# Performance work log

Hardware: AMD Instinct MI355X
Metric: run time of the kernel (lower is better)

The kernel has to match this reference:

```python
import jax, jax.numpy as jnp
import numpy as np

B, L, H, N, NB = 16, 4096, 256, 64, 4
EXPAND = 2


def setup_inputs() -> dict:
    key = jax.random.key(0)
    ks = jax.random.split(key, 12)
    def nrm(k, shape, scale):
        return jax.random.normal(k, shape, dtype=jnp.float32) * scale
    inp = {}
    inp["x"] = jax.random.normal(ks[0], (B, L, 1), dtype=jnp.float32)
    # conv stem: Conv1d(1 -> H, kernel 5, pad 2)
    inp["conv_w"] = nrm(ks[1], (H, 1, 5), 1.0 / np.sqrt(5.0))
    inp["conv_b"] = jnp.zeros((H,), jnp.float32)
    # per-block S4 (S4D diagonal kernel) params, stacked over NB blocks
    inp["s4_norm_w"] = jnp.ones((NB, H), jnp.float32)
    inp["s4_norm_b"] = jnp.zeros((NB, H), jnp.float32)
    inp["log_dt"] = (np.log(0.001) + jax.random.uniform(ks[2], (NB, H), dtype=jnp.float32) * (np.log(0.1) - np.log(0.001))).astype(jnp.float32)
    inp["log_A_real"] = jnp.full((NB, H, N), np.log(0.5), jnp.float32)
    inp["A_imag"] = jnp.tile(np.pi * jnp.arange(N, dtype=jnp.float32), (NB, H, 1))
    inp["C_re"] = nrm(ks[3], (NB, H, N), 0.5 ** 0.5)
    inp["C_im"] = nrm(ks[4], (NB, H, N), 0.5 ** 0.5)
    inp["D"] = nrm(ks[5], (NB, H), 1.0)
    # S4 output GLU linear: H -> 2H, then glu -> H
    inp["s4_out_w"] = nrm(ks[6], (NB, 2 * H, H), 1.0 / np.sqrt(H))
    inp["s4_out_b"] = jnp.zeros((NB, 2 * H), jnp.float32)
    # FF block (expand=2)
    inp["ff_norm_w"] = jnp.ones((NB, H), jnp.float32)
    inp["ff_norm_b"] = jnp.zeros((NB, H), jnp.float32)
    inp["ff_w1"] = nrm(ks[7], (NB, EXPAND * H, H), 1.0 / np.sqrt(H))
    inp["ff_b1"] = jnp.zeros((NB, EXPAND * H), jnp.float32)
    inp["ff_w2"] = nrm(ks[8], (NB, H, EXPAND * H), 1.0 / np.sqrt(EXPAND * H))
    inp["ff_b2"] = jnp.zeros((NB, H), jnp.float32)
    return inp


def _ln_ch(x, w, b):
    # LayerNorm over channel dim of x: [B, H, L] (prenorm on transposed layout)
    mu = jnp.mean(x, axis=1, keepdims=True)
    var = jnp.mean((x - mu) ** 2, axis=1, keepdims=True)
    return (x - mu) * jax.lax.rsqrt(var + 1e-5) * w[None, :, None] + b[None, :, None]


def _s4d_kernel(log_dt, log_A_real, A_imag, C_re, C_im, Lk):
    # Diagonal SSM (S4D) convolution kernel, returns [H, Lk]
    dt = jnp.exp(log_dt)                       # [H]
    A = -jnp.exp(log_A_real) + 1j * A_imag     # [H, N]
    dtA = A * dt[:, None]                      # [H, N]
    C = (C_re + 1j * C_im) * (jnp.exp(dtA) - 1.0) / A
    V = jnp.exp(dtA[:, :, None] * jnp.arange(Lk, dtype=jnp.float32))  # [H, N, Lk]
    return 2.0 * jnp.einsum('hn,hnl->hl', C, V).real


def reference(x, conv_w, conv_b, s4_norm_w, s4_norm_b, log_dt, log_A_real, A_imag,
              C_re, C_im, D, s4_out_w, s4_out_b, ff_norm_w, ff_norm_b,
              ff_w1, ff_b1, ff_w2, ff_b2):
    u = jnp.transpose(x, (0, 2, 1))  # [B, 1, L]
    h = jax.lax.conv_general_dilated(u, conv_w, (1,), [(2, 2)],
                                     dimension_numbers=('NCH', 'OIH', 'NCH'))
    h = h + conv_b[None, :, None]    # [B, H, L]
    Lx = h.shape[-1]
    for i in range(NB):
        # --- S4 residual block (prenorm, FFT long conv, D-skip, GELU, GLU out) ---
        z = _ln_ch(h, s4_norm_w[i], s4_norm_b[i])
        k = _s4d_kernel(log_dt[i], log_A_real[i], A_imag[i], C_re[i], C_im[i], Lx)
        zf = jnp.fft.rfft(z, n=2 * Lx)
        kf = jnp.fft.rfft(k, n=2 * Lx)
        y = jnp.fft.irfft(zf * kf[None], n=2 * Lx)[..., :Lx]
        y = y + z * D[i][None, :, None]
        y = jax.nn.gelu(y, approximate=False)
        y2 = jnp.einsum('fh,bhl->bfl', s4_out_w[i], y) + s4_out_b[i][None, :, None]
        a, g = jnp.split(y2, 2, axis=1)
        h = h + a * jax.nn.sigmoid(g)
        # --- FF residual block (prenorm, pointwise MLP expand=2, GELU) ---
        z = _ln_ch(h, ff_norm_w[i], ff_norm_b[i])
        z = jax.nn.gelu(jnp.einsum('fh,bhl->bfl', ff_w1[i], z) + ff_b1[i][None, :, None], approximate=False)
        z = jnp.einsum('hf,bfl->bhl', ff_w2[i], z) + ff_b2[i][None, :, None]
        h = h + z
    return h[:, :, -1]  # [B, H]
```

## Files before the change

### kernel.cpp

```cpp
#include <hip/hip_runtime.h>
#include <math.h>

#define Bq 16
#define Lq 4096
#define Hq 256
#define Nq 64
#define NBq 4
#define F2q 512
#define BLq (Bq*Lq)

typedef __attribute__((ext_vector_type(8))) short short8;
typedef __attribute__((ext_vector_type(4))) float f32x4;

__device__ __forceinline__ unsigned short f2bf(float f){
  unsigned u = __float_as_uint(f);
  u = (u + 0x7fffu + ((u >> 16) & 1u)) >> 16;
  return (unsigned short)u;
}
__device__ __forceinline__ float bf2f(unsigned short u){
  return __uint_as_float(((unsigned)u) << 16);
}
__device__ __forceinline__ float gelu(float x){
  float u = 0.79788456f*x*(1.f + 0.044715f*x*x);
  float t = 1.f - __fdividef(2.f, 1.f + __expf(2.f*fabsf(u)));
  return 0.5f*x*(1.f + copysignf(t, u));
}

__device__ __forceinline__ void stage16(const void* g, void* l){
  __builtin_amdgcn_global_load_lds((const __attribute__((address_space(1))) void*)g,
                                   (__attribute__((address_space(3))) void*)l, 16, 0, 0);
}

__global__ __launch_bounds__(256) void k_convln(const float* __restrict__ x,
    const float* __restrict__ cw, const float* __restrict__ cb,
    float* __restrict__ h, float* __restrict__ mu, float* __restrict__ rstd){
  __shared__ float xs[260];
  __shared__ float cwS[Hq*5];
  __shared__ float cbS[Hq];
  const int b = blockIdx.x >> 4;
  const int l0 = (blockIdx.x & 15) * 256;
  const int tid = threadIdx.x;
  for (int i=tid; i<Hq*5; i+=256) cwS[i] = cw[i];
  cbS[tid] = cb[tid];
  {
    int gl = l0 + tid - 2;
    xs[tid] = (gl>=0 && gl<Lq) ? x[(size_t)b*Lq + gl] : 0.f;
    if (tid < 4){
      int gl2 = l0 + 254 + tid;
      xs[256+tid] = (gl2>=0 && gl2<Lq) ? x[(size_t)b*Lq + gl2] : 0.f;
    }
  }
  __syncthreads();
  float s0=0.f, s1=0.f;
  float* hp = h + (size_t)b*Hq*Lq + l0 + tid;
  for (int c=0;c<Hq;c++){
    float acc = cbS[c];
    #pragma unroll
    for (int k=0;k<5;k++) acc = fmaf(cwS[c*5+k], xs[tid+k], acc);
    hp[(size_t)c*Lq] = acc;
    s0 += acc; s1 = fmaf(acc, acc, s1);
  }
  int col = b*Lq + l0 + tid;
  float m = s0 * (1.0f/256.0f);
  float var = s1*(1.0f/256.0f) - m*m;
  mu[col] = m;
  rstd[col] = rsqrtf(fmaxf(var, 0.f) + 1e-5f);
}

__global__ __launch_bounds__(256) void k_s4pre(const float* __restrict__ log_dt,
    const float* __restrict__ lar, const float* __restrict__ aim,
    const float* __restrict__ cre, const float* __restrict__ cim,
    float* __restrict__ wre, float* __restrict__ wim,
    float* __restrict__ c2re, float* __restrict__ c2im){
  int idx = blockIdx.x*256 + threadIdx.x;
  int hh = (idx >> 6) & (Hq-1);
  int i = idx >> 14;
  float dt = expf(log_dt[i*Hq + hh]);
  float are = -expf(lar[idx]);
  float ai  = aim[idx];
  float dre = are*dt, dim = ai*dt;
  float er = expf(dre);
  float wr = er*cosf(dim), wi = er*sinf(dim);
  float nr = wr - 1.f, ni = wi;
  float den = are*are + ai*ai;
  float qre = (nr*are + ni*ai)/den;
  float qim = (ni*are - nr*ai)/den;
  float Cr = cre[idx], Ci = cim[idx];
  float cer = Cr*qre - Ci*qim;
  float cei = Cr*qim + Ci*qre;
  wre[idx] = wr; wim[idx] = wi;
  c2re[idx] = 2.f*cer; c2im[idx] = 2.f*cei;
}

__global__ __launch_bounds__(256) void k_cvtw(const float* __restrict__ s0,
    const float* __restrict__ s1, const float* __restrict__ s2,
    unsigned short* __restrict__ d0, unsigned short* __restrict__ d1,
    unsigned short* __restrict__ d2){
  int idx = blockIdx.x*256 + threadIdx.x;
  d0[idx] = f2bf(s0[idx]);
  d1[idx] = f2bf(s1[idx]);
  d2[idx] = f2bf(s2[idx]);
}

__global__ __launch_bounds__(64) void k_s4mat(const float* __restrict__ wre_,
    const float* __restrict__ wim_, const float* __restrict__ c2re_,
    const float* __restrict__ c2im_, const float* __restrict__ Dp,
    unsigned short* __restrict__ G, unsigned short* __restrict__ Wb,
    float* __restrict__ w64re_, float* __restrict__ w64im_){
  __shared__ float Kv[64];
  const int n = threadIdx.x;
  const int ch = blockIdx.x;
  const int pidx = ch*64 + n;
  const float wr = wre_[pidx], wi = wim_[pidx];
  const float cr = c2re_[pidx], ci = c2im_[pidx];
  unsigned short* Gb = G + (size_t)ch*64*192;
  unsigned short* Wbb = Wb + (size_t)ch*128*64;
  float pre = 1.f, pim = 0.f;
  for (int t=0;t<64;t++){
    float a = cr*pre - ci*pim;
    #pragma unroll
    for (int m=1;m<64;m<<=1) a += __shfl_xor(a, m, 64);
    if (n==0) Kv[t] = a;
    Wbb[n*64 + (63-t)] = f2bf(pre);
    Wbb[(64+n)*64 + (63-t)] = f2bf(pim);
    float qre = pre*wr - pim*wi;
    float qim = pre*wi + pim*wr;
    Gb[t*192 + 64 + n]  = f2bf(cr*qre - ci*qim);
    Gb[t*192 + 128 + n] = f2bf(-(cr*qim + ci*qre));
    pre = qre; pim = qim;
  }
  w64re_[pidx] = pre; w64im_[pidx] = pim;
  __syncthreads();
  float dv = Dp[ch];
  for (int t=0;t<64;t++){
    float kv = (n<=t) ? Kv[t-n] : 0.f;
    if (n==t) kv += dv;
    Gb[t*192 + n] = f2bf(kv);
  }
}

__global__ __launch_bounds__(256) void k_lnfin(const float2* __restrict__ stats,
    float* __restrict__ mu, float* __restrict__ rstd){
  int col = blockIdx.x*256 + threadIdx.x;
  float2 s = stats[col];
  float m = s.x * (1.0f/256.0f);
  float var = s.y*(1.0f/256.0f) - m*m;
  mu[col] = m;
  rstd[col] = rsqrtf(fmaxf(var, 0.f) + 1e-5f);
}

__global__ __launch_bounds__(256) void k_prep(const float* __restrict__ h,
    const float* __restrict__ mu, const float* __restrict__ rstd,
    const float* __restrict__ lnw_, const float* __restrict__ lnb_,
    unsigned short* __restrict__ U, int ib){
  int idx = blockIdx.x*256 + threadIdx.x;
  int l = (idx & 511) * 8;
  int ch = (idx >> 9) & (Hq-1);
  int b = idx >> 17;
  float lw = lnw_[ib*Hq+ch], lb = lnb_[ib*Hq+ch];
  const float* hp = h + (((size_t)(b*Hq+ch))<<12) + l;
  const float* mp = mu + ((size_t)b<<12) + l;
  const float* rp = rstd + ((size_t)b<<12) + l;
  unsigned ow[8];
  #pragma unroll
  for (int j=0;j<8;j++){
    float z = (hp[j]-mp[j])*rp[j]*lw + lb;
    ow[j] = f2bf(z);
  }
  uint4 o;
  o.x = ow[0] | (ow[1]<<16); o.y = ow[2] | (ow[3]<<16);
  o.z = ow[4] | (ow[5]<<16); o.w = ow[6] | (ow[7]<<16);
  unsigned short* up = U + ((size_t)ch*1024 + b*64 + (l>>6))*192 + (l&63);
  *(uint4*)up = o;
}

__global__ __launch_bounds__(256,2) void k_bgemm(const unsigned short* __restrict__ Wb,
    const unsigned short* __restrict__ U, unsigned short* __restrict__ Bb){
  __shared__ __align__(16) char smem[34816];
  unsigned short* Alds = (unsigned short*)smem;
  unsigned short* Blds = (unsigned short*)(smem+16384);
  const int tid = threadIdx.x;
  const int lam = tid & 63;
  const int wv = tid >> 6;
  const int wr = wv >> 1, wc = wv & 1;
  const int ch = blockIdx.x;
  const int bc0 = blockIdx.y * 128;
  const unsigned short* Wch = Wb + (size_t)ch*128*64;
  const unsigned short* Uch = U + (size_t)ch*1024*192;
  const int rbase = lam & 15;
  const int kg = lam >> 4;
  const int x7 = lam & 7;
  const int xo0 = ((kg) ^ x7) * 8;
  const int xo1 = ((4+kg) ^ x7) * 8;
  f32x4 acc[4][4] = {};
  #pragma unroll
  for (int c=0;c<4;c++){
    int si = c*256 + tid;
    int row = si >> 3, blk = si & 7;
    int sb = blk ^ (row & 7);
    stage16(Wch + row*64 + sb*8, &Alds[(c*256 + wv*64)*8]);
    stage16(Uch + (size_t)(bc0+row)*192 + sb*8, &Blds[(c*256 + wv*64)*8]);
  }
  __syncthreads();
  #pragma unroll
  for (int kk=0;kk<2;kk++){
    const int xo = kk ? xo1 : xo0;
    short8 af[4], wf[4];
    #pragma unroll
    for (int mf=0;mf<4;mf++)
      af[mf] = *(const short8*)&Alds[(wr*64 + mf*16 + rbase)*64 + xo];
    #pragma unroll
    for (int nf=0;nf<4;nf++)
      wf[nf] = *(const short8*)&Blds[(wc*64 + nf*16 + rbase)*64 + xo];
    #pragma unroll
    for (int mf=0;mf<4;mf++)
      #pragma unroll
      for (int nf=0;nf<4;nf++)
        acc[mf][nf] = __builtin_amdgcn_mfma_f32_16x16x32_bf16(af[mf], wf[nf], acc[mf][nf], 0,0,0);
  }
  __syncthreads();
  unsigned* tru = (unsigned*)smem;
  const int mg = lam >> 4;
  const int ncol = lam & 15;
  #pragma unroll
  for (int nf=0;nf<4;nf++){
    int bcl = wc*64 + nf*16 + ncol;
    #pragma unroll
    for (int mf=0;mf<4;mf++){
      int n2h = wr*32 + mf*8 + mg*2;
      tru[bcl*68 + n2h]     = (unsigned)f2bf(acc[mf][nf][0]) | ((unsigned)f2bf(acc[mf][nf][1])<<16);
      tru[bcl*68 + n2h + 1] = (unsigned)f2bf(acc[mf][nf][2]) | ((unsigned)f2bf(acc[mf][nf][3])<<16);
    }
  }
  __syncthreads();
  {
    int row = tid >> 1, half = tid & 1;
    const unsigned* src = tru + row*68 + half*32;
    unsigned short* dst = Bb + ((size_t)ch*1024 + bc0 + row)*128 + half*64;
    #pragma unroll
    for (int j=0;j<8;j++)
      *(uint4*)(dst + j*8) = *(const uint4*)(src + j*4);
  }
}

__global__ __launch_bounds__(256) void k_cscan(const unsigned short* __restrict__ Bb,
    const float* __restrict__ w64re_, const float* __restrict__ w64im_,
    unsigned short* __restrict__ U){
  const int wid = blockIdx.x*4 + (threadIdx.x >> 6);
  const int n = threadIdx.x & 63;
  const int ch = wid & (Hq-1);
  const int b = wid >> 8;
  const float wr = w64re_[ch*64 + n];
  const float wi = w64im_[ch*64 + n];
  const unsigned short* bp = Bb + ((size_t)ch*1024 + b*64)*128 + n;
  unsigned short* up = U + ((size_t)ch*1024 + b*64)*192;
  float sre = 0.f, sim = 0.f;
  for (int c=0;c<64;c++){
    up[c*192 + 64 + n]  = f2bf(sre);
    up[c*192 + 128 + n] = f2bf(sim);
    float br = bf2f(bp[c*128]), bi = bf2f(bp[c*128 + 64]);
    float t = fmaf(wr, sre, fmaf(-wi, sim, br));
    sim = fmaf(wr, sim, fmaf(wi, sre, bi));
    sre = t;
  }
}

__global__ __launch_bounds__(256,2) void k_ygemm(const unsigned short* __restrict__ G,
    const unsigned short* __restrict__ U, unsigned short* __restrict__ ybuf){
  __shared__ __align__(16) char smem[40960];
  unsigned short* Alds = (unsigned short*)smem;
  unsigned short* Blds = (unsigned short*)(smem + 8192);
  const int tid = threadIdx.x;
  const int lam = tid & 63;
  const int wv = tid >> 6;
  const int ch = blockIdx.x;
  const int col0 = blockIdx.y * 256;
  const unsigned short* Gch = G + (size_t)ch*64*192;
  const unsigned short* Uch = U + (size_t)ch*1024*192;
  const int rbase = lam & 15;
  const int kg = lam >> 4;
  const int x7 = lam & 7;
  const int xo0 = ((kg) ^ x7) * 8;
  const int xo1 = ((4+kg) ^ x7) * 8;
  f32x4 acc[4][4] = {};
  for (int ks=0;ks<3;ks++){
    const int k0 = ks*64;
    #pragma unroll
    for (int c=0;c<2;c++){
      int si = c*256 + tid;
      int row = si >> 3, blk = si & 7;
      int sb = blk ^ (row & 7);
      stage16(Gch + row*192 + k0 + sb*8, &Alds[(c*256 + wv*64)*8]);
    }
    #pragma unroll
    for (int c=0;c<8;c++){
      int si = c*256 + tid;
      int row = si >> 3, blk = si & 7;
      int sb = blk ^ (row & 7);
      stage16(Uch + (size_t)(col0+row)*192 + k0 + sb*8, &Blds[(c*256 + wv*64)*8]);
    }
    __syncthreads();
    #pragma unroll
    for (int kk=0;kk<2;kk++){
      const int xo = kk ? xo1 : xo0;
      short8 af[4], wf[4];
      #pragma unroll
      for (int mf=0;mf<4;mf++)
        af[mf] = *(const short8*)&Alds[(mf*16 + rbase)*64 + xo];
      #pragma unroll
      for (int nf=0;nf<4;nf++)
        wf[nf] = *(const short8*)&Blds[(wv*64 + nf*16 + rbase)*64 + xo];
      #pragma unroll
      for (int mf=0;mf<4;mf++)
        #pragma unroll
        for (int nf=0;nf<4;nf++)
          acc[mf][nf] = __builtin_amdgcn_mfma_f32_16x16x32_bf16(af[mf], wf[nf], acc[mf][nf], 0,0,0);
    }
    __syncthreads();
  }
  unsigned short* trans = (unsigned short*)smem + wv*64*66;
  const int mg = lam >> 4;
  const int ncol = lam & 15;
  #pragma unroll
  for (int mf=0;mf<4;mf++){
    #pragma unroll
    for (int nf=0;nf<4;nf++){
      #pragma unroll
      for (int r=0;r<4;r++){
        int l = mf*16 + mg*4 + r;
        int bcl = nf*16 + ncol;
        trans[bcl*66 + l] = f2bf(gelu(acc[mf][nf][r]));
      }
    }
  }
  __syncthreads();
  const int bc = col0 + wv*64 + lam;
  const int b = bc >> 6, c = bc & 63;
  unsigned short* yp = ybuf + (((size_t)(b*Hq + ch))<<12) + c*64;
  #pragma unroll
  for (int j=0;j<8;j++){
    uint4 v = *(const uint4*)&trans[lam*66 + j*8];
    *(uint4*)(yp + j*8) = v;
  }
}

__global__ __launch_bounds__(256) void k_transp(const unsigned short* __restrict__ src,
    unsigned short* __restrict__ dst){
  __shared__ unsigned lds[64][65];
  const int t = threadIdx.x;
  const int tile = blockIdx.x;
  const int l0 = (tile & 63)*64;
  const int c0 = ((tile>>6)&3)*64;
  const int b = tile >> 8;
  const int rr = t >> 3, c8 = t & 7;
  #pragma unroll
  for (int q=0;q<2;q++){
    int ch = rr + q*32;
    const unsigned short* sp = src + ((size_t)b*Hq + c0+ch)*Lq + l0 + c8*8;
    uint4 v = *(const uint4*)sp;
    lds[ch][c8*8+0] = v.x & 0xffff; lds[ch][c8*8+1] = v.x >> 16;
    lds[ch][c8*8+2] = v.y & 0xffff; lds[ch][c8*8+3] = v.y >> 16;
    lds[ch][c8*8+4] = v.z & 0xffff; lds[ch][c8*8+5] = v.z >> 16;
    lds[ch][c8*8+6] = v.w & 0xffff; lds[ch][c8*8+7] = v.w >> 16;
  }
  __syncthreads();
  #pragma unroll
  for (int q=0;q<2;q++){
    int l = rr + q*32;
    unsigned a[8];
    #pragma unroll
    for (int j=0;j<8;j++) a[j] = lds[c8*8+j][l];
    uint4 o;
    o.x = (a[0]&0xffff) | (a[1]<<16);
    o.y = (a[2]&0xffff) | (a[3]<<16);
    o.z = (a[4]&0xffff) | (a[5]<<16);
    o.w = (a[6]&0xffff) | (a[7]<<16);
    *(uint4*)(dst + ((size_t)b*Lq + l0+l)*Hq + c0 + c8*8) = o;
  }
}

__global__ __launch_bounds__(256) void k_lntransp(const float* __restrict__ h,
    const float* __restrict__ mu, const float* __restrict__ rstd,
    const float* __restrict__ lnw_, const float* __restrict__ lnb_,
    unsigned short* __restrict__ dst, int ib){
  __shared__ unsigned lds[64][65];
  const int t = threadIdx.x;
  const int tile = blockIdx.x;
  const int l0 = (tile & 63)*64;
  const int c0 = ((tile>>6)&3)*64;
  const int b = tile >> 8;
  const int rr = t >> 3, c8 = t & 7;
  #pragma unroll
  for (int q=0;q<2;q++){
    int ch = c0 + rr + q*32;
    float lw = lnw_[ib*Hq + ch], lb = lnb_[ib*Hq + ch];
    const float* sp = h + ((size_t)b*Hq + ch)*Lq + l0 + c8*8;
    const float* mp = mu + (size_t)b*Lq + l0 + c8*8;
    const float* rp = rstd + (size_t)b*Lq + l0 + c8*8;
    #pragma unroll
    for (int j=0;j<8;j++){
      float z = (sp[j] - mp[j]) * rp[j] * lw + lb;
      lds[rr + q*32][c8*8+j] = f2bf(z);
    }
  }
  __syncthreads();
  #pragma unroll
  for (int q=0;q<2;q++){
    int l = rr + q*32;
    unsigned a[8];
    #pragma unroll
    for (int j=0;j<8;j++) a[j] = lds[c8*8+j][l];
    uint4 o;
    o.x = (a[0]&0xffff) | (a[1]<<16);
    o.y = (a[2]&0xffff) | (a[3]<<16);
    o.z = (a[4]&0xffff) | (a[5]<<16);
    o.w = (a[6]&0xffff) | (a[7]<<16);
    *(uint4*)(dst + ((size_t)b*Lq + l0+l)*Hq + c0 + c8*8) = o;
  }
}

template<int MODE, int KDIM>
__global__ __launch_bounds__(256,2) void k_gemm(
    const unsigned short* __restrict__ A, const unsigned short* __restrict__ W,
    const float* __restrict__ bias, float* __restrict__ h,
    unsigned short* __restrict__ out, float2* __restrict__ stats){
  constexpr int WSH = (MODE==0?2:1)*128*64;
  constexpr int SMEM_MAIN = (128*64 + WSH)*2;
  constexpr int SMEM = (MODE==1 && SMEM_MAIN < 34816) ? 34816 : SMEM_MAIN;
  __shared__ __align__(16) char smem[SMEM];
  unsigned short* Alds = (unsigned short*)smem;
  unsigned short* Wlds = Alds + 128*64;
  const int tid = threadIdx.x;
  const int lam = tid & 63;
  const int wv = tid >> 6;
  const int wr = wv >> 1, wc = wv & 1;
  const int col0 = blockIdx.x * 128;
  const int n0 = blockIdx.y * 128;
  const int rbase = lam & 15;
  const int kg = lam >> 4;
  const int x7 = lam & 7;
  const int xo0 = ((kg) ^ x7) * 8;
  const int xo1 = ((4+kg) ^ x7) * 8;
  const unsigned short *aP[4], *wP[4], *wP2[4];
  unsigned sDst[4];
  #pragma unroll
  for (int c=0;c<4;c++){
    int si = c*256 + tid;
    int row = si >> 3, blk = si & 7;
    int sb = blk ^ (row & 7);
    aP[c] = A + (size_t)(col0+row)*KDIM + sb*8;
    wP[c] = W + (size_t)(n0+row)*KDIM + sb*8;
    wP2[c] = (MODE==0) ? (W + (size_t)(n0+256+row)*KDIM + sb*8) : nullptr;
    sDst[c] = (unsigned)(c*256 + wv*64)*8;
  }
  f32x4 acc[4][4] = {};
  f32x4 acc2[4][4] = {};
  for (int k0 = 0; k0 < KDIM; k0 += 64){
    #pragma unroll
    for (int c=0;c<4;c++){
      stage16(aP[c] + k0, &Alds[sDst[c]]);
      stage16(wP[c] + k0, &Wlds[sDst[c]]);
      if constexpr (MODE==0) stage16(wP2[c] + k0, &Wlds[8192 + sDst[c]]);
    }
    __syncthreads();
    #pragma unroll
    for (int kk=0;kk<2;kk++){
      const int xo = kk ? xo1 : xo0;
      short8 af[4], wf[4];
      #pragma unroll
      for (int mf=0;mf<4;mf++)
        af[mf] = *(const short8*)&Alds[(wr*64 + mf*16 + rbase)*64 + xo];
      #pragma unroll
      for (int nf=0;nf<4;nf++)
        wf[nf] = *(const short8*)&Wlds[(wc*64 + nf*16 + rbase)*64 + xo];
      if constexpr (MODE==0){
        short8 wg[4];
        #pragma unroll
        for (int nf=0;nf<4;nf++)
          wg[nf] = *(const short8*)&Wlds[8192 + (wc*64 + nf*16 + rbase)*64 + xo];
        #pragma unroll
        for (int mf=0;mf<4;mf++){
          #pragma unroll
          for (int nf=0;nf<4;nf++){
            acc[mf][nf]  = __builtin_amdgcn_mfma_f32_16x16x32_bf16(af[mf], wf[nf], acc[mf][nf], 0,0,0);
            acc2[mf][nf] = __builtin_amdgcn_mfma_f32_16x16x32_bf16(af[mf], wg[nf], acc2[mf][nf], 0,0,0);
          }
        }
      } else {
        #pragma unroll
        for (int mf=0;mf<4;mf++){
          #pragma unroll
          for (int nf=0;nf<4;nf++)
            acc[mf][nf] = __builtin_amdgcn_mfma_f32_16x16x32_bf16(af[mf], wf[nf], acc[mf][nf], 0,0,0);
        }
      }
    }
    __syncthreads();
  }
  const int mg = lam >> 4;
  const int ncol = lam & 15;
  if constexpr (MODE==1){
    unsigned short* trans = (unsigned short*)smem;
    #pragma unroll
    for (int nf=0;nf<4;nf++){
      int gnl = wc*64 + nf*16 + ncol;
      float bb1 = bias[n0 + gnl];
      #pragma unroll
      for (int mf=0;mf<4;mf++){
        int cl = wr*64 + mf*16 + mg*4;
        #pragma unroll
        for (int r=0;r<4;r++)
          trans[(cl+r)*136 + gnl] = f2bf(gelu(acc[mf][nf][r] + bb1));
      }
    }
    __syncthreads();
    {
      int cl = tid >> 1, gs = (tid & 1)*64;
      const unsigned short* src = trans + cl*136 + gs;
      unsigned short* dst = out + (size_t)(col0+cl)*F2q + n0 + gs;
      #pragma unroll
      for (int j=0;j<8;j++)
        *(uint4*)(dst + j*8) = *(const uint4*)(src + j*8);
    }
  } else {
    float s0a[4][4] = {};
    float s1a[4][4] = {};
    #pragma unroll
    for (int nf=0;nf<4;nf++){
      int gn = n0 + wc*64 + nf*16 + ncol;
      float ba = bias[gn];
      float bg = (MODE==0) ? bias[gn + Hq] : 0.f;
      #pragma unroll
      for (int mf=0;mf<4;mf++){
        int gcol = col0 + wr*64 + mf*16 + mg*4;
        int bb = gcol >> 12, ll = gcol & (Lq-1);
        float* hp = h + ((size_t)bb*Hq + gn)*Lq + ll;
        f32x4 hv = *(f32x4*)hp;
        #pragma unroll
        for (int r=0;r<4;r++){
          if constexpr (MODE==0){
            float av = acc[mf][nf][r] + ba;
            float gv = acc2[mf][nf][r] + bg;
            hv[r] += __fdividef(av, 1.f + __expf(-gv));
          } else {
            hv[r] += acc[mf][nf][r] + ba;
          }
          s0a[mf][r] += hv[r];
          s1a[mf][r] = fmaf(hv[r], hv[r], s1a[mf][r]);
        }
        *(f32x4*)hp = hv;
      }
    }
    #pragma unroll
    for (int mf=0;mf<4;mf++){
      #pragma unroll
      for (int r=0;r<4;r++){
        float v0 = s0a[mf][r], v1 = s1a[mf][r];
        #pragma unroll
        for (int m=1;m<16;m<<=1){
          v0 += __shfl_xor(v0, m, 64);
          v1 += __shfl_xor(v1, m, 64);
        }
        if (ncol == 0){
          int row = col0 + wr*64 + mf*16 + mg*4 + r;
          atomicAdd(&stats[row].x, v0);
          atomicAdd(&stats[row].y, v1);
        }
      }
    }
  }
}

__global__ __launch_bounds__(256) void k_gather(const float* __restrict__ h,
    float* __restrict__ o){
  int idx = blockIdx.x*256 + threadIdx.x;
  int b = idx >> 8, c = idx & (Hq-1);
  o[idx] = h[((size_t)b*Hq + c)*Lq + (Lq-1)];
}

extern "C" void kernel_launch(void* const* d_in, const int* in_sizes, int n_in,
                              void* d_out, int out_size, void* d_ws, size_t ws_size,
                              hipStream_t stream) {
  (void)in_sizes; (void)n_in; (void)out_size; (void)ws_size;
  const float* x         = (const float*)d_in[0];
  const float* conv_w    = (const float*)d_in[1];
  const float* conv_b    = (const float*)d_in[2];
  const float* s4_norm_w = (const float*)d_in[3];
  const float* s4_norm_b = (const float*)d_in[4];
  const float* log_dt    = (const float*)d_in[5];
  const float* log_A_real= (const float*)d_in[6];
  const float* A_imag    = (const float*)d_in[7];
  const float* C_re      = (const float*)d_in[8];
  const float* C_im      = (const float*)d_in[9];
  const float* Dp        = (const float*)d_in[10];
  const float* s4_out_w  = (const float*)d_in[11];
  const float* s4_out_b  = (const float*)d_in[12];
  const float* ff_norm_w = (const float*)d_in[13];
  const float* ff_norm_b = (const float*)d_in[14];
  const float* ff_w1     = (const float*)d_in[15];
  const float* ff_b1     = (const float*)d_in[16];
  const float* ff_w2     = (const float*)d_in[17];
  const float* ff_b2     = (const float*)d_in[18];

  char* ws = (char*)d_ws;
  size_t off = 0;
  auto nxt = [&](size_t bytes){ size_t o = off; off = (off + bytes + 255) & ~(size_t)255; return o; };
  float* h      = (float*)(ws + nxt((size_t)Bq*Hq*Lq*4));
  float* mu     = (float*)(ws + nxt((size_t)BLq*4));
  float* rstd   = (float*)(ws + nxt((size_t)BLq*4));
  float* wre    = (float*)(ws + nxt((size_t)NBq*Hq*Nq*4));
  float* wim    = (float*)(ws + nxt((size_t)NBq*Hq*Nq*4));
  float* c2re   = (float*)(ws + nxt((size_t)NBq*Hq*Nq*4));
  float* c2im   = (float*)(ws + nxt((size_t)NBq*Hq*Nq*4));
  float* w64re  = (float*)(ws + nxt((size_t)NBq*Hq*Nq*4));
  float* w64im  = (float*)(ws + nxt((size_t)NBq*Hq*Nq*4));
  unsigned short* s4wb = (unsigned short*)(ws + nxt((size_t)NBq*F2q*Hq*2));
  unsigned short* f1b  = (unsigned short*)(ws + nxt((size_t)NBq*F2q*Hq*2));
  unsigned short* f2b  = (unsigned short*)(ws + nxt((size_t)NBq*Hq*F2q*2));
  unsigned short* Gm   = (unsigned short*)(ws + nxt((size_t)Hq*64*192*2));
  unsigned short* Wbar = (unsigned short*)(ws + nxt((size_t)Hq*128*64*2));
  unsigned short* U    = (unsigned short*)(ws + nxt((size_t)Hq*1024*192*2));
  unsigned short* Bb   = (unsigned short*)(ws + nxt((size_t)Hq*128*1024*2));
  unsigned short* ybuf = Bb;
  unsigned short* yT   = Bb + (size_t)16*1024*1024;
  unsigned short* zT   = yT;
  unsigned short* z2T  = U;
  float2* stats = (float2*)Bb;

  k_convln<<<Bq*16, 256, 0, stream>>>(x, conv_w, conv_b, h, mu, rstd);
  k_s4pre<<<(NBq*Hq*Nq)/256, 256, 0, stream>>>(log_dt, log_A_real, A_imag, C_re, C_im,
                                               wre, wim, c2re, c2im);
  k_cvtw<<<(NBq*F2q*Hq)/256, 256, 0, stream>>>(s4_out_w, ff_w1, ff_w2, s4wb, f1b, f2b);

  for (int i=0;i<NBq;i++){
    const size_t po = (size_t)i*Hq*Nq;
    k_s4mat<<<Hq, 64, 0, stream>>>(wre+po, wim+po, c2re+po, c2im+po, Dp + i*Hq,
                                   Gm, Wbar, w64re+po, w64im+po);
    k_prep<<<(Bq*Hq*Lq/8)/256, 256, 0, stream>>>(h, mu, rstd, s4_norm_w, s4_norm_b, U, i);
    k_bgemm<<<dim3(Hq, 8), 256, 0, stream>>>(Wbar, U, Bb);
    k_cscan<<<(Bq*Hq)/4, 256, 0, stream>>>(Bb, w64re+po, w64im+po, U);
    k_ygemm<<<dim3(Hq, 4), 256, 0, stream>>>(Gm, U, ybuf);
    k_transp<<<Bq*4*64, 256, 0, stream>>>(ybuf, yT);
    hipMemsetAsync(stats, 0, (size_t)BLq*sizeof(float2), stream);
    k_gemm<0,256><<<dim3(BLq/128, 2), 256, 0, stream>>>(
        yT, s4wb + (size_t)i*F2q*Hq, s4_out_b + (size_t)i*F2q, h, nullptr, stats);
    k_lnfin<<<BLq/256, 256, 0, stream>>>(stats, mu, rstd);
    k_lntransp<<<Bq*4*64, 256, 0, stream>>>(h, mu, rstd, ff_norm_w, ff_norm_b, zT, i);
    k_gemm<1,256><<<dim3(BLq/128, 4), 256, 0, stream>>>(
        zT, f1b + (size_t)i*F2q*Hq, ff_b1 + (size_t)i*F2q, nullptr, z2T, nullptr);
    hipMemsetAsync(stats, 0, (size_t)BLq*sizeof(float2), stream);
    k_gemm<2,512><<<dim3(BLq/128, 2), 256, 0, stream>>>(
        z2T, f2b + (size_t)i*Hq*F2q, ff_b2 + (size_t)i*Hq, h, nullptr, stats);
    k_lnfin<<<BLq/256, 256, 0, stream>>>(stats, mu, rstd);
  }
  k_gather<<<(Bq*Hq)/256, 256, 0, stream>>>(h, (float*)d_out);
}
```

Baseline: 1.341 ms.

## Store residual stream channel-last and fuse FF LayerNorm into first FF GEMM

Switches the fp32 residual buffer h from [B,H,L] to a [B*L,H] token-major layout. The conv stem, prep, GEMM epilogues and gather are rewritten to match: epilogues stage results through LDS so the residual update and row stats are coalesced, with one atomic pair per row. The separate LayerNorm+transpose kernel before the first FF GEMM is removed, and that GEMM now normalizes fp32 rows into bf16 LDS tiles itself. This saves a full activation pass per block, but the FF1 GEMM does its A-loads synchronously in registers instead of async LDS loads, and k_prep must now transpose through LDS.

```diff
diff --git a/kernel.cpp b/kernel.cpp
--- a/kernel.cpp
+++ b/kernel.cpp
@@ -33,38 +33,51 @@
 
 __global__ __launch_bounds__(256) void k_convln(const float* __restrict__ x,
     const float* __restrict__ cw, const float* __restrict__ cb,
-    float* __restrict__ h, float* __restrict__ mu, float* __restrict__ rstd){
-  __shared__ float xs[260];
+    float* __restrict__ hT, float* __restrict__ mu, float* __restrict__ rstd){
   __shared__ float cwS[Hq*5];
   __shared__ float cbS[Hq];
-  const int b = blockIdx.x >> 4;
-  const int l0 = (blockIdx.x & 15) * 256;
-  const int tid = threadIdx.x;
-  for (int i=tid; i<Hq*5; i+=256) cwS[i] = cw[i];
-  cbS[tid] = cb[tid];
-  {
-    int gl = l0 + tid - 2;
-    xs[tid] = (gl>=0 && gl<Lq) ? x[(size_t)b*Lq + gl] : 0.f;
-    if (tid < 4){
-      int gl2 = l0 + 254 + tid;
-      xs[256+tid] = (gl2>=0 && gl2<Lq) ? x[(size_t)b*Lq + gl2] : 0.f;
-    }
-  }
-  __syncthreads();
+  __shared__ float xs[20];
+  const int b = blockIdx.x >> 8;
+  const int l0 = (blockIdx.x & 255) * 16;
+  const int t = threadIdx.x;
+  const int chg = (t & 15) * 16;
+  const int ll  = t >> 4;
+  for (int i=t; i<Hq*5; i+=256) cwS[i] = cw[i];
+  cbS[t] = cb[t];
+  if (t < 20){
+    int gl = l0 + t - 2;
+    xs[t] = (gl>=0 && gl<Lq) ? x[(size_t)b*Lq + gl] : 0.f;
+  }
+  __syncthreads();
+  float xv[5];
+  #pragma unroll
+  for (int k=0;k<5;k++) xv[k] = xs[ll+k];
   float s0=0.f, s1=0.f;
-  float* hp = h + (size_t)b*Hq*Lq + l0 + tid;
-  for (int c=0;c<Hq;c++){
+  float ov[16];
+  #pragma unroll
+  for (int j=0;j<16;j++){
+    int c = chg + j;
     float acc = cbS[c];
     #pragma unroll
-    for (int k=0;k<5;k++) acc = fmaf(cwS[c*5+k], xs[tid+k], acc);
-    hp[(size_t)c*Lq] = acc;
+    for (int k=0;k<5;k++) acc = fmaf(cwS[c*5+k], xv[k], acc);
+    ov[j] = acc;
     s0 += acc; s1 = fmaf(acc, acc, s1);
   }
-  int col = b*Lq + l0 + tid;
-  float m = s0 * (1.0f/256.0f);
-  float var = s1*(1.0f/256.0f) - m*m;
-  mu[col] = m;
-  rstd[col] = rsqrtf(fmaxf(var, 0.f) + 1e-5f);
+  float* hp = hT + ((size_t)(b*Lq + l0 + ll))*Hq + chg;
+  #pragma unroll
+  for (int j=0;j<4;j++) *(f32x4*)(hp + j*4) = *(f32x4*)&ov[j*4];
+  #pragma unroll
+  for (int m=1;m<16;m<<=1){
+    s0 += __shfl_xor(s0, m, 64);
+    s1 += __shfl_xor(s1, m, 64);
+  }
+  if ((t & 15) == 0){
+    int col = b*Lq + l0 + ll;
+    float m = s0 * (1.0f/256.0f);
+    float var = s1*(1.0f/256.0f) - m*m;
+    mu[col] = m;
+    rstd[col] = rsqrtf(fmaxf(var, 0.f) + 1e-5f);
+  }
 }
 
 __global__ __launch_bounds__(256) void k_s4pre(const float* __restrict__ log_dt,
@@ -149,29 +162,39 @@
   rstd[col] = rsqrtf(fmaxf(var, 0.f) + 1e-5f);
 }
 
-__global__ __launch_bounds__(256) void k_prep(const float* __restrict__ h,
+__global__ __launch_bounds__(256) void k_prep(const float* __restrict__ hT,
     const float* __restrict__ mu, const float* __restrict__ rstd,
     const float* __restrict__ lnw_, const float* __restrict__ lnb_,
     unsigned short* __restrict__ U, int ib){
-  int idx = blockIdx.x*256 + threadIdx.x;
-  int l = (idx & 511) * 8;
-  int ch = (idx >> 9) & (Hq-1);
-  int b = idx >> 17;
-  float lw = lnw_[ib*Hq+ch], lb = lnb_[ib*Hq+ch];
-  const float* hp = h + (((size_t)(b*Hq+ch))<<12) + l;
-  const float* mp = mu + ((size_t)b<<12) + l;
-  const float* rp = rstd + ((size_t)b<<12) + l;
-  unsigned ow[8];
-  #pragma unroll
-  for (int j=0;j<8;j++){
-    float z = (hp[j]-mp[j])*rp[j]*lw + lb;
-    ow[j] = f2bf(z);
-  }
-  uint4 o;
-  o.x = ow[0] | (ow[1]<<16); o.y = ow[2] | (ow[3]<<16);
-  o.z = ow[4] | (ow[5]<<16); o.w = ow[6] | (ow[7]<<16);
-  unsigned short* up = U + ((size_t)ch*1024 + b*64 + (l>>6))*192 + (l&63);
-  *(uint4*)up = o;
+  __shared__ unsigned short trans[64*72];
+  const int bid = blockIdx.x;
+  const int b = bid >> 8;
+  const int lt = (bid >> 2) & 63;
+  const int ct = bid & 3;
+  const int l0 = lt*64, ch0 = ct*64;
+  const int t = threadIdx.x;
+  {
+    const int lloc = t >> 2;
+    const int cc = (t & 3) * 16;
+    const int gcol = b*Lq + l0 + lloc;
+    const float* hp = hT + (size_t)gcol*Hq + ch0 + cc;
+    float muv = mu[gcol], rsv = rstd[gcol];
+    const float* lw = lnw_ + ib*Hq + ch0 + cc;
+    const float* lb = lnb_ + ib*Hq + ch0 + cc;
+    #pragma unroll
+    for (int j=0;j<16;j++){
+      float z = (hp[j]-muv)*rsv*lw[j] + lb[j];
+      trans[(cc+j)*72 + lloc] = f2bf(z);
+    }
+  }
+  __syncthreads();
+  {
+    const int c = t >> 2, seg = t & 3;
+    unsigned short* dst = U + ((size_t)(ch0+c)*1024 + b*64 + lt)*192 + seg*16;
+    const unsigned short* src = trans + c*72 + seg*16;
+    *(uint4*)dst = *(const uint4*)src;
+    *(uint4*)(dst+8) = *(const uint4*)(src+8);
+  }
 }
 
 __global__ __launch_bounds__(256,2) void k_bgemm(const unsigned short* __restrict__ Wb,
@@ -379,57 +402,21 @@
   }
 }
 
-__global__ __launch_bounds__(256) void k_lntransp(const float* __restrict__ h,
-    const float* __restrict__ mu, const float* __restrict__ rstd,
-    const float* __restrict__ lnw_, const float* __restrict__ lnb_,
-    unsigned short* __restrict__ dst, int ib){
-  __shared__ unsigned lds[64][65];
-  const int t = threadIdx.x;
-  const int tile = blockIdx.x;
-  const int l0 = (tile & 63)*64;
-  const int c0 = ((tile>>6)&3)*64;
-  const int b = tile >> 8;
-  const int rr = t >> 3, c8 = t & 7;
-  #pragma unroll
-  for (int q=0;q<2;q++){
-    int ch = c0 + rr + q*32;
-    float lw = lnw_[ib*Hq + ch], lb = lnb_[ib*Hq + ch];
-    const float* sp = h + ((size_t)b*Hq + ch)*Lq + l0 + c8*8;
-    const float* mp = mu + (size_t)b*Lq + l0 + c8*8;
-    const float* rp = rstd + (size_t)b*Lq + l0 + c8*8;
-    #pragma unroll
-    for (int j=0;j<8;j++){
-      float z = (sp[j] - mp[j]) * rp[j] * lw + lb;
-      lds[rr + q*32][c8*8+j] = f2bf(z);
-    }
-  }
-  __syncthreads();
-  #pragma unroll
-  for (int q=0;q<2;q++){
-    int l = rr + q*32;
-    unsigned a[8];
-    #pragma unroll
-    for (int j=0;j<8;j++) a[j] = lds[c8*8+j][l];
-    uint4 o;
-    o.x = (a[0]&0xffff) | (a[1]<<16);
-    o.y = (a[2]&0xffff) | (a[3]<<16);
-    o.z = (a[4]&0xffff) | (a[5]<<16);
-    o.w = (a[6]&0xffff) | (a[7]<<16);
-    *(uint4*)(dst + ((size_t)b*Lq + l0+l)*Hq + c0 + c8*8) = o;
-  }
-}
-
 template<int MODE, int KDIM>
 __global__ __launch_bounds__(256,2) void k_gemm(
-    const unsigned short* __restrict__ A, const unsigned short* __restrict__ W,
-    const float* __restrict__ bias, float* __restrict__ h,
-    unsigned short* __restrict__ out, float2* __restrict__ stats){
-  constexpr int WSH = (MODE==0?2:1)*128*64;
-  constexpr int SMEM_MAIN = (128*64 + WSH)*2;
-  constexpr int SMEM = (MODE==1 && SMEM_MAIN < 34816) ? 34816 : SMEM_MAIN;
+    const void* __restrict__ Ap, const unsigned short* __restrict__ W,
+    const float* __restrict__ bias, float* __restrict__ hT,
+    unsigned short* __restrict__ out, float2* __restrict__ stats,
+    const float* __restrict__ mu, const float* __restrict__ rstd,
+    const float* __restrict__ lnw_, const float* __restrict__ lnb_){
+  constexpr int ASTG = 128*64;
+  constexpr int WSTG = (MODE==0?2:1)*128*64;
+  constexpr int STG_B = (ASTG+WSTG)*2 + (MODE==1 ? 2048 : 0);
+  constexpr int EPI_B = (MODE==1) ? 128*136*2 : 128*132*4;
+  constexpr int SMEM = STG_B > EPI_B ? STG_B : EPI_B;
   __shared__ __align__(16) char smem[SMEM];
   unsigned short* Alds = (unsigned short*)smem;
-  unsigned short* Wlds = Alds + 128*64;
+  unsigned short* Wlds = Alds + ASTG;
   const int tid = threadIdx.x;
   const int lam = tid & 63;
   const int wv = tid >> 6;
@@ -441,26 +428,61 @@
   const int x7 = lam & 7;
   const int xo0 = ((kg) ^ x7) * 8;
   const int xo1 = ((4+kg) ^ x7) * 8;
-  const unsigned short *aP[4], *wP[4], *wP2[4];
+  const unsigned short *wP[4], *wP2[4];
   unsigned sDst[4];
+  const unsigned short* aPb[4];
   #pragma unroll
   for (int c=0;c<4;c++){
     int si = c*256 + tid;
     int row = si >> 3, blk = si & 7;
     int sb = blk ^ (row & 7);
-    aP[c] = A + (size_t)(col0+row)*KDIM + sb*8;
     wP[c] = W + (size_t)(n0+row)*KDIM + sb*8;
     wP2[c] = (MODE==0) ? (W + (size_t)(n0+256+row)*KDIM + sb*8) : nullptr;
+    aPb[c] = (MODE!=1) ? ((const unsigned short*)Ap + (size_t)(col0+row)*KDIM + sb*8) : nullptr;
     sDst[c] = (unsigned)(c*256 + wv*64)*8;
+  }
+  float* lnS = (float*)(smem + (ASTG+WSTG)*2);
+  float muv = 0.f, rsv = 0.f;
+  const float* hrow = nullptr;
+  if constexpr (MODE==1){
+    lnS[tid] = lnw_[tid];
+    lnS[256+tid] = lnb_[tid];
+    int arow = tid >> 1;
+    muv = mu[col0 + arow];
+    rsv = rstd[col0 + arow];
+    hrow = (const float*)Ap + (size_t)(col0 + arow)*Hq + (tid&1)*32;
+    __syncthreads();
   }
   f32x4 acc[4][4] = {};
   f32x4 acc2[4][4] = {};
   for (int k0 = 0; k0 < KDIM; k0 += 64){
-    #pragma unroll
-    for (int c=0;c<4;c++){
-      stage16(aP[c] + k0, &Alds[sDst[c]]);
-      stage16(wP[c] + k0, &Wlds[sDst[c]]);
-      if constexpr (MODE==0) stage16(wP2[c] + k0, &Wlds[8192 + sDst[c]]);
+    if constexpr (MODE==1){
+      const int arow = tid >> 1;
+      const int kbb = (tid & 1)*4;
+      #pragma unroll
+      for (int j=0;j<4;j++){
+        f32x4 v0 = *(const f32x4*)(hrow + k0 + j*8);
+        f32x4 v1 = *(const f32x4*)(hrow + k0 + j*8 + 4);
+        int chg = k0 + (tid&1)*32 + j*8;
+        short8 pk;
+        #pragma unroll
+        for (int e=0;e<4;e++){
+          float z0 = (v0[e]-muv)*rsv*lnS[chg+e] + lnS[256+chg+e];
+          float z1 = (v1[e]-muv)*rsv*lnS[chg+4+e] + lnS[256+chg+4+e];
+          pk[e] = (short)f2bf(z0);
+          pk[4+e] = (short)f2bf(z1);
+        }
+        *(short8*)&Alds[arow*64 + ((kbb+j)^(arow&7))*8] = pk;
+      }
+      #pragma unroll
+      for (int c=0;c<4;c++) stage16(wP[c] + k0, &Wlds[sDst[c]]);
+    } else {
+      #pragma unroll
+      for (int c=0;c<4;c++){
+        stage16(aPb[c] + k0, &Alds[sDst[c]]);
+        stage16(wP[c] + k0, &Wlds[sDst[c]]);
+        if constexpr (MODE==0) stage16(wP2[c] + k0, &Wlds[8192 + sDst[c]]);
+      }
     }
     __syncthreads();
     #pragma unroll
@@ -523,59 +545,65 @@
         *(uint4*)(dst + j*8) = *(const uint4*)(src + j*8);
     }
   } else {
-    float s0a[4][4] = {};
-    float s1a[4][4] = {};
+    float* dlds = (float*)smem;
     #pragma unroll
     for (int nf=0;nf<4;nf++){
-      int gn = n0 + wc*64 + nf*16 + ncol;
+      int chl = wc*64 + nf*16 + ncol;
+      int gn = n0 + chl;
       float ba = bias[gn];
       float bg = (MODE==0) ? bias[gn + Hq] : 0.f;
       #pragma unroll
       for (int mf=0;mf<4;mf++){
-        int gcol = col0 + wr*64 + mf*16 + mg*4;
-        int bb = gcol >> 12, ll = gcol & (Lq-1);
-        float* hp = h + ((size_t)bb*Hq + gn)*Lq + ll;
-        f32x4 hv = *(f32x4*)hp;
+        int cl = wr*64 + mf*16 + mg*4;
         #pragma unroll
         for (int r=0;r<4;r++){
+          float d;
           if constexpr (MODE==0){
             float av = acc[mf][nf][r] + ba;
             float gv = acc2[mf][nf][r] + bg;
-            hv[r] += __fdividef(av, 1.f + __expf(-gv));
+            d = __fdividef(av, 1.f + __expf(-gv));
           } else {
-            hv[r] += acc[mf][nf][r] + ba;
+            d = acc[mf][nf][r] + ba;
           }
-          s0a[mf][r] += hv[r];
-          s1a[mf][r] = fmaf(hv[r], hv[r], s1a[mf][r]);
+          dlds[(cl+r)*132 + chl] = d;
         }
-        *(f32x4*)hp = hv;
-      }
-    }
-    #pragma unroll
-    for (int mf=0;mf<4;mf++){
-      #pragma unroll
-      for (int r=0;r<4;r++){
-        float v0 = s0a[mf][r], v1 = s1a[mf][r];
-        #pragma unroll
-        for (int m=1;m<16;m<<=1){
-          v0 += __shfl_xor(v0, m, 64);
-          v1 += __shfl_xor(v1, m, 64);
+      }
+    }
+    __syncthreads();
+    {
+      const int row = tid >> 1;
+      const int ce = (tid & 1)*64;
+      const int gcol = col0 + row;
+      float* hp = hT + (size_t)gcol*Hq + n0 + ce;
+      const float* dp = dlds + row*132 + ce;
+      float s0 = 0.f, s1 = 0.f;
+      #pragma unroll
+      for (int j=0;j<16;j++){
+        f32x4 hv = *(f32x4*)(hp + j*4);
+        f32x4 dv = *(const f32x4*)(dp + j*4);
+        #pragma unroll
+        for (int r=0;r<4;r++){
+          hv[r] += dv[r];
+          s0 += hv[r];
+          s1 = fmaf(hv[r], hv[r], s1);
         }
-        if (ncol == 0){
-          int row = col0 + wr*64 + mf*16 + mg*4 + r;
-          atomicAdd(&stats[row].x, v0);
-          atomicAdd(&stats[row].y, v1);
-        }
-      }
-    }
-  }
-}
-
-__global__ __launch_bounds__(256) void k_gather(const float* __restrict__ h,
+        *(f32x4*)(hp + j*4) = hv;
+      }
+      s0 += __shfl_xor(s0, 1, 64);
+      s1 += __shfl_xor(s1, 1, 64);
+      if (!(tid & 1)){
+        atomicAdd(&stats[gcol].x, s0);
+        atomicAdd(&stats[gcol].y, s1);
+      }
+    }
+  }
+}
+
+__global__ __launch_bounds__(256) void k_gather(const float* __restrict__ hT,
     float* __restrict__ o){
   int idx = blockIdx.x*256 + threadIdx.x;
   int b = idx >> 8, c = idx & (Hq-1);
-  o[idx] = h[((size_t)b*Hq + c)*Lq + (Lq-1)];
+  o[idx] = hT[((size_t)(b*Lq + Lq-1))*Hq + c];
 }
 
 extern "C" void kernel_launch(void* const* d_in, const int* in_sizes, int n_in,
@@ -605,7 +633,7 @@
   char* ws = (char*)d_ws;
   size_t off = 0;
   auto nxt = [&](size_t bytes){ size_t o = off; off = (off + bytes + 255) & ~(size_t)255; return o; };
-  float* h      = (float*)(ws + nxt((size_t)Bq*Hq*Lq*4));
+  float* hT     = (float*)(ws + nxt((size_t)Bq*Lq*Hq*4));
   float* mu     = (float*)(ws + nxt((size_t)BLq*4));
   float* rstd   = (float*)(ws + nxt((size_t)BLq*4));
   float* wre    = (float*)(ws + nxt((size_t)NBq*Hq*Nq*4));
@@ -623,11 +651,10 @@
   unsigned short* Bb   = (unsigned short*)(ws + nxt((size_t)Hq*128*1024*2));
   unsigned short* ybuf = Bb;
   unsigned short* yT   = Bb + (size_t)16*1024*1024;
-  unsigned short* zT   = yT;
   unsigned short* z2T  = U;
   float2* stats = (float2*)Bb;
 
-  k_convln<<<Bq*16, 256, 0, stream>>>(x, conv_w, conv_b, h, mu, rstd);
+  k_convln<<<Bq*256, 256, 0, stream>>>(x, conv_w, conv_b, hT, mu, rstd);
   k_s4pre<<<(NBq*Hq*Nq)/256, 256, 0, stream>>>(log_dt, log_A_real, A_imag, C_re, C_im,
                                                wre, wim, c2re, c2im);
   k_cvtw<<<(NBq*F2q*Hq)/256, 256, 0, stream>>>(s4_out_w, ff_w1, ff_w2, s4wb, f1b, f2b);
@@ -636,22 +663,24 @@
     const size_t po = (size_t)i*Hq*Nq;
     k_s4mat<<<Hq, 64, 0, stream>>>(wre+po, wim+po, c2re+po, c2im+po, Dp + i*Hq,
                                    Gm, Wbar, w64re+po, w64im+po);
-    k_prep<<<(Bq*Hq*Lq/8)/256, 256, 0, stream>>>(h, mu, rstd, s4_norm_w, s4_norm_b, U, i);
+    k_prep<<<Bq*256, 256, 0, stream>>>(hT, mu, rstd, s4_norm_w, s4_norm_b, U, i);
     k_bgemm<<<dim3(Hq, 8), 256, 0, stream>>>(Wbar, U, Bb);
     k_cscan<<<(Bq*Hq)/4, 256, 0, stream>>>(Bb, w64re+po, w64im+po, U);
     k_ygemm<<<dim3(Hq, 4), 256, 0, stream>>>(Gm, U, ybuf);
     k_transp<<<Bq*4*64, 256, 0, stream>>>(ybuf, yT);
     hipMemsetAsync(stats, 0, (size_t)BLq*sizeof(float2), stream);
     k_gemm<0,256><<<dim3(BLq/128, 2), 256, 0, stream>>>(
-        yT, s4wb + (size_t)i*F2q*Hq, s4_out_b + (size_t)i*F2q, h, nullptr, stats);
+        yT, s4wb + (size_t)i*F2q*Hq, s4_out_b + (size_t)i*F2q, hT, nullptr, stats,
+        nullptr, nullptr, nullptr, nullptr);
     k_lnfin<<<BLq/256, 256, 0, stream>>>(stats, mu, rstd);
-    k_lntransp<<<Bq*4*64, 256, 0, stream>>>(h, mu, rstd, ff_norm_w, ff_norm_b, zT, i);
     k_gemm<1,256><<<dim3(BLq/128, 4), 256, 0, stream>>>(
-        zT, f1b + (size_t)i*F2q*Hq, ff_b1 + (size_t)i*F2q, nullptr, z2T, nullptr);
+        hT, f1b + (size_t)i*F2q*Hq, ff_b1 + (size_t)i*F2q, nullptr, z2T, nullptr,
+        mu, rstd, ff_norm_w + (size_t)i*Hq, ff_norm_b + (size_t)i*Hq);
     hipMemsetAsync(stats, 0, (size_t)BLq*sizeof(float2), stream);
     k_gemm<2,512><<<dim3(BLq/128, 2), 256, 0, stream>>>(
-        z2T, f2b + (size_t)i*Hq*F2q, ff_b2 + (size_t)i*Hq, h, nullptr, stats);
+        z2T, f2b + (size_t)i*Hq*F2q, ff_b2 + (size_t)i*Hq, hT, nullptr, stats,
+        nullptr, nullptr, nullptr, nullptr);
     k_lnfin<<<BLq/256, 256, 0, stream>>>(stats, mu, rstd);
   }
-  k_gather<<<(Bq*Hq)/256, 256, 0, stream>>>(h, (float*)d_out);
-}
+  k_gather<<<(Bq*Hq)/256, 256, 0, stream>>>(hT, (float*)d_out);
+}
```

New measurement: 1.471 ms. 1.1x slower.

## Stage GEMM epilogue through LDS for coalesced residual update and stats

Applied to the files above, without the earlier changes.

The residual-add epilogue of the GEMM now writes its per-fragment deltas into shared memory. Each 64-channel half is then read back so that threads update h with contiguous 128-byte row segments instead of scattered 16-byte accesses. Per-column LayerNorm statistics are computed from the LDS copy with a short shuffle rather than a 16-lane butterfly. This adds three barriers per half and makes the shared buffer larger, which may lower occupancy for the MODE 0 variant.

```diff
diff --git a/kernel.cpp b/kernel.cpp
--- a/kernel.cpp
+++ b/kernel.cpp
@@ -425,8 +425,9 @@
     const float* __restrict__ bias, float* __restrict__ h,
     unsigned short* __restrict__ out, float2* __restrict__ stats){
   constexpr int WSH = (MODE==0?2:1)*128*64;
-  constexpr int SMEM_MAIN = (128*64 + WSH)*2;
-  constexpr int SMEM = (MODE==1 && SMEM_MAIN < 34816) ? 34816 : SMEM_MAIN;
+  constexpr int STG_B = (128*64 + WSH)*2;
+  constexpr int EPI_B = (MODE==1) ? 128*136*2 : 64*132*4;
+  constexpr int SMEM = STG_B > EPI_B ? STG_B : EPI_B;
   __shared__ __align__(16) char smem[SMEM];
   unsigned short* Alds = (unsigned short*)smem;
   unsigned short* Wlds = Alds + 128*64;
@@ -523,48 +524,66 @@
         *(uint4*)(dst + j*8) = *(const uint4*)(src + j*8);
     }
   } else {
-    float s0a[4][4] = {};
-    float s1a[4][4] = {};
-    #pragma unroll
-    for (int nf=0;nf<4;nf++){
-      int gn = n0 + wc*64 + nf*16 + ncol;
-      float ba = bias[gn];
-      float bg = (MODE==0) ? bias[gn + Hq] : 0.f;
-      #pragma unroll
-      for (int mf=0;mf<4;mf++){
-        int gcol = col0 + wr*64 + mf*16 + mg*4;
-        int bb = gcol >> 12, ll = gcol & (Lq-1);
-        float* hp = h + ((size_t)bb*Hq + gn)*Lq + ll;
-        f32x4 hv = *(f32x4*)hp;
-        #pragma unroll
-        for (int r=0;r<4;r++){
-          if constexpr (MODE==0){
-            float av = acc[mf][nf][r] + ba;
-            float gv = acc2[mf][nf][r] + bg;
-            hv[r] += __fdividef(av, 1.f + __expf(-gv));
-          } else {
-            hv[r] += acc[mf][nf][r] + ba;
+    float* dlds = (float*)smem;
+    const int bb = col0 >> 12;
+    const int l0 = col0 & (Lq-1);
+    #pragma unroll
+    for (int p=0;p<2;p++){
+      __syncthreads();
+      if (wc == p){
+        #pragma unroll
+        for (int nf=0;nf<4;nf++){
+          int chl = nf*16 + ncol;
+          int gn = n0 + p*64 + chl;
+          float ba = bias[gn];
+          float bg = (MODE==0) ? bias[gn + Hq] : 0.f;
+          #pragma unroll
+          for (int mf=0;mf<4;mf++){
+            int coll = wr*64 + mf*16 + mg*4;
+            #pragma unroll
+            for (int r=0;r<4;r++){
+              float d;
+              if constexpr (MODE==0){
+                float av = acc[mf][nf][r] + ba;
+                float gv = acc2[mf][nf][r] + bg;
+                d = __fdividef(av, 1.f + __expf(-gv));
+              } else {
+                d = acc[mf][nf][r] + ba;
+              }
+              dlds[chl*132 + coll + r] = d;
+            }
           }
-          s0a[mf][r] += hv[r];
-          s1a[mf][r] = fmaf(hv[r], hv[r], s1a[mf][r]);
         }
-        *(f32x4*)hp = hv;
       }
-    }
-    #pragma unroll
-    for (int mf=0;mf<4;mf++){
-      #pragma unroll
-      for (int r=0;r<4;r++){
-        float v0 = s0a[mf][r], v1 = s1a[mf][r];
-        #pragma unroll
-        for (int m=1;m<16;m<<=1){
-          v0 += __shfl_xor(v0, m, 64);
-          v1 += __shfl_xor(v1, m, 64);
+      __syncthreads();
+      {
+        int chl = tid >> 2, lq = (tid & 3)*32;
+        float* hp = h + ((size_t)bb*Hq + n0 + p*64 + chl)*Lq + l0 + lq;
+        float* dp = dlds + chl*132 + lq;
+        #pragma unroll
+        for (int j=0;j<8;j++){
+          f32x4 hv = *(f32x4*)(hp + j*4);
+          f32x4 dv = *(const f32x4*)(dp + j*4);
+          #pragma unroll
+          for (int r=0;r<4;r++) hv[r] += dv[r];
+          *(f32x4*)(hp + j*4) = hv;
+          *(f32x4*)(dp + j*4) = hv;
         }
-        if (ncol == 0){
-          int row = col0 + wr*64 + mf*16 + mg*4 + r;
-          atomicAdd(&stats[row].x, v0);
-          atomicAdd(&stats[row].y, v1);
+      }
+      __syncthreads();
+      {
+        int j = tid >> 1, hc = (tid & 1)*32;
+        float s0 = 0.f, s1 = 0.f;
+        #pragma unroll
+        for (int c=0;c<32;c++){
+          float v = dlds[(hc+c)*132 + j];
+          s0 += v; s1 = fmaf(v, v, s1);
+        }
+        s0 += __shfl_xor(s0, 1, 64);
+        s1 += __shfl_xor(s1, 1, 64);
+        if (!(tid & 1)){
+          atomicAdd(&stats[col0 + j].x, s0);
+          atomicAdd(&stats[col0 + j].y, s1);
         }
       }
     }
```

After: 1.333 ms. No clear change (-0.6%).
